# Kernel optimization log

Hardware: AMD Instinct MI355X
Metric: run time of the kernel (lower is better)

The kernel has to match this reference:

```python
import jax, jax.numpy as jnp
import numpy as np

EPS = 1e-05


def layer_norm(x, scale):
    # Faithful to source bug: returns scale * x_norm + scale (shift param unused)
    mean = jnp.mean(x, axis=-1, keepdims=True)
    var = jnp.var(x, axis=-1, keepdims=True)  # unbiased=False
    x_norm = (x - mean) / jnp.sqrt(var + EPS)
    return scale * x_norm + scale


def mhsa(x, wq, wk, wv, wo, bo, n_heads):
    b, t, d = x.shape
    hd = d // n_heads
    # torch Linear: y = x @ W.T (no qkv bias)
    q = (x @ wq.T).reshape(b, t, n_heads, hd).transpose(0, 2, 1, 3)  # bhtd
    k = (x @ wk.T).reshape(b, t, n_heads, hd).transpose(0, 2, 1, 3)
    v = (x @ wv.T).reshape(b, t, n_heads, hd).transpose(0, 2, 1, 3)
    scores = jnp.einsum('bhqd,bhkd->bhqk', q, k)
    causal = jnp.triu(jnp.ones((t, t), dtype=bool), k=1)
    scores = jnp.where(causal, -jnp.inf, scores)
    attn = jax.nn.softmax(scores / np.sqrt(hd).astype(np.float32), axis=-1)
    ctx = jnp.einsum('bhqk,bhkd->bhqd', attn, v)
    ctx = ctx.transpose(0, 2, 1, 3).reshape(b, t, d)
    return ctx @ wo.T + bo


def setup_inputs() -> dict:
    key = jax.random.key(0)
    ks = jax.random.split(key, 6)
    B, T, D = 2, 2048, 1024
    return {
        'x': jax.random.normal(ks[0], (B, T, D), dtype=jnp.float32),
        'wq': jax.random.normal(ks[1], (D, D), dtype=jnp.float32) * 0.02,
        'wk': jax.random.normal(ks[2], (D, D), dtype=jnp.float32) * 0.02,
        'wv': jax.random.normal(ks[3], (D, D), dtype=jnp.float32) * 0.02,
        'wo': jax.random.normal(ks[4], (D, D), dtype=jnp.float32) * 0.02,
        'bo': jnp.zeros((D,), dtype=jnp.float32),
        'ln1_scale': jnp.ones((D,), dtype=jnp.float32),
        'ln2_scale': jnp.ones((D,), dtype=jnp.float32),
    }


def reference(x, wq, wk, wv, wo, bo, ln1_scale, ln2_scale):
    n_heads = 16
    # Block 1: norm1 -> attn -> (+residual); dropout is identity in eval mode
    h = x + mhsa(layer_norm(x, ln1_scale), wq, wk, wv, wo, bo, n_heads)
    # Block 2: source calls self.attn (same weights) again, not self.ff
    out = h + mhsa(layer_norm(h, ln2_scale), wq, wk, wv, wo, bo, n_heads)
    return out
```

## Files before the change

### kernel.cpp

```cpp
#include <hip/hip_runtime.h>
#include <hip/hip_bf16.h>
#include <math.h>

#define Dm 1024
#define Tm 2048
#define Bm 2
#define Hm 16
#define HDm 64
#define Rm (Bm*Tm)
#define QKS 2048

typedef __attribute__((ext_vector_type(8))) short sh8;
typedef __attribute__((ext_vector_type(4))) float f32x4;
typedef __attribute__((ext_vector_type(16))) float f32x16;

#define AS1(p) ((const __attribute__((address_space(1))) void*)(p))
#define AS3(p) ((__attribute__((address_space(3))) void*)(p))

__device__ __forceinline__ short f2bs(float f) {
    union { float f; unsigned u; } v; v.f = f;
    unsigned r = v.u + 0x7FFFu + ((v.u >> 16) & 1u);
    return (short)(r >> 16);
}

__global__ __launch_bounds__(256) void convert_w(const float* __restrict__ wq,
                                                 const float* __restrict__ wk,
                                                 const float* __restrict__ wv,
                                                 const float* __restrict__ wo,
                                                 short* __restrict__ wqkv,
                                                 short* __restrict__ wob) {
    int idx = (blockIdx.x * 256 + threadIdx.x) * 4;
    const int M1 = 1 << 20;
    const float* src; short* dst; int off; float sc = 1.0f;
    if (idx < M1)           { src = wq; dst = wqkv;          off = idx; sc = 0.125f; }
    else if (idx < 2*M1)    { src = wk; dst = wqkv + M1;     off = idx - M1; }
    else if (idx < 3*M1)    { src = wv; dst = wqkv + 2*M1;   off = idx - 2*M1; }
    else                    { src = wo; dst = wob;           off = idx - 3*M1; }
    float4 v = *(const float4*)(src + off);
    short4 o;
    o.x = f2bs(v.x*sc); o.y = f2bs(v.y*sc); o.z = f2bs(v.z*sc); o.w = f2bs(v.w*sc);
    *(short4*)(dst + off) = o;
}

__global__ __launch_bounds__(256) void ln_kernel(const float* __restrict__ x,
                                                 const float* __restrict__ scale,
                                                 short* __restrict__ out) {
    int row = blockIdx.x;
    int t = threadIdx.x;
    const float4* xr = (const float4*)(x + (size_t)row * Dm);
    float4 v = xr[t];
    float s  = v.x + v.y + v.z + v.w;
    float ss = v.x*v.x + v.y*v.y + v.z*v.z + v.w*v.w;
    #pragma unroll
    for (int off = 32; off; off >>= 1) {
        s  += __shfl_xor(s, off);
        ss += __shfl_xor(ss, off);
    }
    __shared__ float red[8];
    int wave = t >> 6, lane = t & 63;
    if (lane == 0) { red[wave*2] = s; red[wave*2+1] = ss; }
    __syncthreads();
    s  = red[0] + red[2] + red[4] + red[6];
    ss = red[1] + red[3] + red[5] + red[7];
    float mean = s * (1.0f / Dm);
    float var  = ss * (1.0f / Dm) - mean * mean;
    float rstd = 1.0f / sqrtf(var + 1e-5f);
    float4 sc = ((const float4*)scale)[t];
    short4 o;
    o.x = f2bs(sc.x * ((v.x - mean) * rstd) + sc.x);
    o.y = f2bs(sc.y * ((v.y - mean) * rstd) + sc.y);
    o.z = f2bs(sc.z * ((v.z - mean) * rstd) + sc.z);
    o.w = f2bs(sc.w * ((v.w - mean) * rstd) + sc.w);
    ((short4*)(out + (size_t)row * Dm))[t] = o;
}

template<int BN, int MODE>
__global__ __launch_bounds__(256) void gemm_mfma(const short* __restrict__ A,
                                                 const short* __restrict__ B,
                                                 const float* __restrict__ bias,
                                                 const float* __restrict__ res,
                                                 void* __restrict__ Cv,
                                                 short* __restrict__ Vt,
                                                 int M, int N, int K) {
    __shared__ short As[128*32];
    __shared__ short Bs[BN*32];
    __shared__ short Tb[(MODE==1) ? 4*16*68 : 4];
    const int NJ = BN / 32;
    int t = threadIdx.x;
    int lane = t & 63, w = t >> 6;
    int l = lane & 15, quad = lane >> 4;
    int wm = (w & 1) * 64, wn = (w >> 1) * (BN/2);
    int m0 = blockIdx.y * 128, n0 = blockIdx.x * BN;

    f32x4 acc[4][NJ];
    #pragma unroll
    for (int i = 0; i < 4; i++)
        #pragma unroll
        for (int j = 0; j < NJ; j++)
            acc[i][j] = (f32x4){0.f,0.f,0.f,0.f};

    for (int k0 = 0; k0 < K; k0 += 32) {
        __syncthreads();
        #pragma unroll
        for (int p = 0; p < 2; p++) {
            int off = p*4096 + t*16;
            int row = off >> 6;
            int c = ((off >> 4) & 3) ^ (row & 3);
            const short* ga = A + (size_t)(m0 + row) * K + k0 + c*8;
            __builtin_amdgcn_global_load_lds(AS1(ga), AS3((char*)As + off), 16, 0, 0);
        }
        #pragma unroll
        for (int p = 0; p < BN/64; p++) {
            int off = p*4096 + t*16;
            int row = off >> 6;
            int c = ((off >> 4) & 3) ^ (row & 3);
            const short* gb = B + (size_t)(n0 + row) * K + k0 + c*8;
            __builtin_amdgcn_global_load_lds(AS1(gb), AS3((char*)Bs + off), 16, 0, 0);
        }
        __syncthreads();
        sh8 af[4], bf[NJ];
        #pragma unroll
        for (int i = 0; i < 4; i++) {
            int m = wm + i*16 + l;
            af[i] = *(const sh8*)((const char*)As + m*64 + ((quad ^ (m & 3)) * 16));
        }
        #pragma unroll
        for (int j = 0; j < NJ; j++) {
            int n = wn + j*16 + l;
            bf[j] = *(const sh8*)((const char*)Bs + n*64 + ((quad ^ (n & 3)) * 16));
        }
        #pragma unroll
        for (int i = 0; i < 4; i++)
            #pragma unroll
            for (int j = 0; j < NJ; j++)
                acc[i][j] = __builtin_amdgcn_mfma_f32_16x16x32_bf16(af[i], bf[j], acc[i][j], 0, 0, 0);
    }
    if (MODE == 0) {
        #pragma unroll
        for (int i = 0; i < 4; i++)
            #pragma unroll
            for (int j = 0; j < NJ; j++)
                #pragma unroll
                for (int r = 0; r < 4; r++) {
                    int m = m0 + wm + i*16 + quad*4 + r;
                    int n = n0 + wn + j*16 + l;
                    float vv = acc[i][j][r] + bias[n] + res[(size_t)m * N + n];
                    ((float*)Cv)[(size_t)m * N + n] = vv;
                }
    } else {
        if (n0 < 2048) {
            #pragma unroll
            for (int i = 0; i < 4; i++)
                #pragma unroll
                for (int j = 0; j < NJ; j++)
                    #pragma unroll
                    for (int r = 0; r < 4; r++) {
                        int m = m0 + wm + i*16 + quad*4 + r;
                        int n = n0 + wn + j*16 + l;
                        ((short*)Cv)[(size_t)m * QKS + n] = f2bs(acc[i][j][r]);
                    }
        } else {
            int bq = m0 >> 11;
            int key0 = (m0 & 2047) + wm;
            int h = (n0 + wn - 2048) >> 6;
            int quad2 = ((quad & 1) << 1) | (quad >> 1);
            short* vout = Vt + ((size_t)(bq*Hm + h) * HDm) * Tm + key0;
            #pragma unroll
            for (int j = 0; j < NJ; j++) {
                #pragma unroll
                for (int i = 0; i < 4; i++) {
                    short4 o;
                    o.x = f2bs(acc[i][j][0]); o.y = f2bs(acc[i][j][1]);
                    o.z = f2bs(acc[i][j][2]); o.w = f2bs(acc[i][j][3]);
                    *(short4*)&Tb[w*(16*68) + l*68 + i*16 + quad2*4] = o;
                }
                #pragma unroll
                for (int st = 0; st < 2; st++) {
                    int rr = st*8 + (lane >> 3);
                    int cc = lane & 7;
                    sh8 vv = *(const sh8*)&Tb[w*(16*68) + rr*68 + cc*8];
                    *(sh8*)(vout + (size_t)(j*16 + rr) * Tm + cc*8) = vv;
                }
            }
        }
    }
}

__global__ __launch_bounds__(256) void attn_mfma(const short* __restrict__ qk,
                                                 const short* __restrict__ vtg,
                                                 short* __restrict__ ctx) {
    __shared__ short Kl[3][64*64];
    __shared__ short Vl[2][64*64];
    int t = threadIdx.x;
    int lane = t & 63, w = t >> 6;
    int qh = w & 1, kh = w >> 1;
    int l31 = lane & 31, hi = lane >> 5;
    int bh = blockIdx.x;
    int xi = blockIdx.y;
    int cc0 = xi & 7, kk0 = xi >> 3;
    int qt = (kk0 == 0) ? cc0 : (kk0 == 1) ? (15 - cc0)
           : (kk0 == 2) ? (16 + cc0) : (31 - cc0);
    int b = bh >> 4, h = bh & 15;
    size_t rbase = (size_t)b * Tm;
    const short* qp0 = qk + rbase * QKS + h*HDm;
    const short* kp0 = qp0 + Dm;
    const short* vh  = vtg + ((size_t)bh * HDm) * Tm;
    int qtbase = qt * 64;
    int qrow = qtbase + qh*32 + l31;

    sh8 qf[4];
    {
        const short* qp = qp0 + (size_t)qrow * QKS + hi*8;
        qf[0] = *(const sh8*)qp;
        qf[1] = *(const sh8*)(qp + 16);
        qf[2] = *(const sh8*)(qp + 32);
        qf[3] = *(const sh8*)(qp + 48);
    }

    f32x16 O0, O1;
    #pragma unroll
    for (int i = 0; i < 16; i++) { O0[i] = 0.f; O1[i] = 0.f; }
    float ps = 0.f;

    int trow = t >> 3;
    int c8 = ((t & 7) ^ (trow & 7)) * 8;
    int ldsoff = t * 16;
    const short* gkp = kp0 + (size_t)trow * QKS + c8;
    const short* gvp = vh + (size_t)trow * Tm + c8;

#define STAGE_K(KD) do { \
    __builtin_amdgcn_global_load_lds(AS1(gkp),                  AS3((char*)(KD) + ldsoff), 16, 0, 0); \
    __builtin_amdgcn_global_load_lds(AS1(gkp + (size_t)32*QKS), AS3((char*)(KD) + 4096 + ldsoff), 16, 0, 0); \
    gkp += (size_t)64*QKS; } while (0)

#define STAGE_V(VD) do { \
    __builtin_amdgcn_global_load_lds(AS1(gvp),                 AS3((char*)(VD) + ldsoff), 16, 0, 0); \
    __builtin_amdgcn_global_load_lds(AS1(gvp + (size_t)32*Tm), AS3((char*)(VD) + 4096 + ldsoff), 16, 0, 0); \
    gvp += 64; } while (0)

#define QKCOMP(KBUF) do { \
    const char* kr_ = (const char*)(KBUF) + (kh*32 + l31)*128; \
    int sw_ = l31 & 7; \
    f32x16 c_; \
    _Pragma("unroll") for (int i_ = 0; i_ < 16; i_++) c_[i_] = 0.f; \
    _Pragma("unroll") for (int s_ = 0; s_ < 4; s_++) { \
        sh8 kf_ = *(const sh8*)(kr_ + (((s_*2 + hi) ^ sw_) * 16)); \
        c_ = __builtin_amdgcn_mfma_f32_32x32x16_bf16(kf_, qf[s_], c_, 0, 0, 0); } \
    S0 = c_; \
} while (0)

    STAGE_K(Kl[0]);
    STAGE_V(Vl[0]);
    if (qt >= 1) STAGE_K(Kl[1]);
    __syncthreads();

    f32x16 S0;
    QKCOMP(Kl[0]);

    int bcur = 0;
    for (int kc = 0; kc <= qt; kc++) {
        int kbase = kc * 64;
        sh8 pa[2];
        {
            bool needmask = (kbase + kh*32 + 31 > qtbase + qh*32);
            float p_[16];
            if (needmask) {
                #pragma unroll
                for (int r = 0; r < 16; r++) {
                    int key_r = kbase + kh*32 + (r&3) + 8*(r>>2) + 4*hi;
                    p_[r] = (key_r > qrow) ? 0.f : __expf(S0[r]);
                }
            } else {
                #pragma unroll
                for (int r = 0; r < 16; r++) p_[r] = __expf(S0[r]);
            }
            ps += (((p_[0]+p_[1])+(p_[2]+p_[3])) + ((p_[4]+p_[5])+(p_[6]+p_[7])))
                + (((p_[8]+p_[9])+(p_[10]+p_[11])) + ((p_[12]+p_[13])+(p_[14]+p_[15])));
            #pragma unroll
            for (int gg = 0; gg < 2; gg++) {
                union { __hip_bfloat162 h2[4]; sh8 s8; } u;
                u.h2[0] = __float22bfloat162_rn({p_[gg*8+0], p_[gg*8+1]});
                u.h2[1] = __float22bfloat162_rn({p_[gg*8+2], p_[gg*8+3]});
                u.h2[2] = __float22bfloat162_rn({p_[gg*8+4], p_[gg*8+5]});
                u.h2[3] = __float22bfloat162_rn({p_[gg*8+6], p_[gg*8+7]});
                pa[gg] = u.s8;
            }
        }

        __syncthreads();

        int bnext = (bcur == 2) ? 0 : bcur + 1;
        if (kc + 2 <= qt) {
            int bnext2 = (bnext == 2) ? 0 : bnext + 1;
            STAGE_K(Kl[bnext2]);
        }
        if (kc + 1 <= qt) STAGE_V(Vl[(kc + 1) & 1]);

        if (kc < qt) QKCOMP(Kl[bnext]);

        const char* Vb = (const char*)Vl[kc & 1];
        int G0 = kh * 2;
        {
            const char* vr = Vb + l31*128;
            int sw = l31 & 7;
            sh8 v0 = *(const sh8*)(vr + ((((G0  )*2 + hi) ^ sw) * 16));
            sh8 v1 = *(const sh8*)(vr + ((((G0+1)*2 + hi) ^ sw) * 16));
            O0 = __builtin_amdgcn_mfma_f32_32x32x16_bf16(pa[0], v0, O0, 0, 0, 0);
            O0 = __builtin_amdgcn_mfma_f32_32x32x16_bf16(pa[1], v1, O0, 0, 0, 0);
        }
        {
            const char* vr = Vb + (32 + l31)*128;
            int sw = l31 & 7;
            sh8 v0 = *(const sh8*)(vr + ((((G0  )*2 + hi) ^ sw) * 16));
            sh8 v1 = *(const sh8*)(vr + ((((G0+1)*2 + hi) ^ sw) * 16));
            O1 = __builtin_amdgcn_mfma_f32_32x32x16_bf16(pa[0], v0, O1, 0, 0, 0);
            O1 = __builtin_amdgcn_mfma_f32_32x32x16_bf16(pa[1], v1, O1, 0, 0, 0);
        }
        bcur = bnext;
    }
#undef STAGE_K
#undef STAGE_V
#undef QKCOMP

    ps += __shfl_xor(ps, 32);
    __syncthreads();
    float* Lo  = (float*)Kl;
    float* Lps = (float*)Vl;
    if (kh == 1) {
        #pragma unroll
        for (int r = 0; r < 16; r++) {
            int rl = (r&3) + 8*(r>>2) + 4*hi;
            Lo[qh*2048 + rl*64 + l31]      = O0[r];
            Lo[qh*2048 + rl*64 + 32 + l31] = O1[r];
        }
        if (hi == 0) Lps[qh*32 + l31] = ps;
    }
    __syncthreads();
    if (kh == 0) {
        float pst = ps + Lps[qh*32 + l31];
        float inv_own = 1.0f / pst;
        short* cp = ctx + (rbase + qtbase + qh*32) * Dm + h*HDm + l31;
        #pragma unroll
        for (int r = 0; r < 16; r++) {
            int rl = (r&3) + 8*(r>>2) + 4*hi;
            float inv = __shfl(inv_own, rl);
            cp[(size_t)rl * Dm]      = f2bs((O0[r] + Lo[qh*2048 + rl*64 + l31]) * inv);
            cp[(size_t)rl * Dm + 32] = f2bs((O1[r] + Lo[qh*2048 + rl*64 + 32 + l31]) * inv);
        }
    }
}

extern "C" void kernel_launch(void* const* d_in, const int* in_sizes, int n_in,
                              void* d_out, int out_size, void* d_ws, size_t ws_size,
                              hipStream_t stream) {
    const float* x   = (const float*)d_in[0];
    const float* wq  = (const float*)d_in[1];
    const float* wk  = (const float*)d_in[2];
    const float* wv  = (const float*)d_in[3];
    const float* wo  = (const float*)d_in[4];
    const float* bo  = (const float*)d_in[5];
    const float* ln1 = (const float*)d_in[6];
    const float* ln2 = (const float*)d_in[7];
    float* out = (float*)d_out;

    short* lnb  = (short*)d_ws;
    short* ctxb = lnb  + (size_t)Rm*Dm;
    short* qk   = ctxb + (size_t)Rm*Dm;
    short* vtg  = qk   + (size_t)Rm*QKS;
    short* wqkv = vtg  + (size_t)Bm*Hm*HDm*Tm;
    short* wob  = wqkv + (size_t)3*Dm*Dm;

    dim3 qgrid(3072/128, Rm/128);
    dim3 pgrid(Dm/64,    Rm/128);
    dim3 agrid(32, 32);

    convert_w<<<4096, 256, 0, stream>>>(wq, wk, wv, wo, wqkv, wob);

    ln_kernel<<<Rm, 256, 0, stream>>>(x, ln1, lnb);
    gemm_mfma<128, 1><<<qgrid, 256, 0, stream>>>(lnb, wqkv, nullptr, nullptr, qk, vtg, Rm, 3072, Dm);
    attn_mfma<<<agrid, 256, 0, stream>>>(qk, vtg, ctxb);
    gemm_mfma<64, 0><<<pgrid, 256, 0, stream>>>(ctxb, wob, bo, x, out, nullptr, Rm, Dm, Dm);

    ln_kernel<<<Rm, 256, 0, stream>>>(out, ln2, lnb);
    gemm_mfma<128, 1><<<qgrid, 256, 0, stream>>>(lnb, wqkv, nullptr, nullptr, qk, vtg, Rm, 3072, Dm);
    attn_mfma<<<agrid, 256, 0, stream>>>(qk, vtg, ctxb);
    gemm_mfma<64, 0><<<pgrid, 256, 0, stream>>>(ctxb, wob, bo, out, out, nullptr, Rm, Dm, Dm);
}
```

Measured before the change: 284.6 us.

## Double GEMM K-tile to 64 and fuse weight conversion into first layernorm

Each GEMM k-step now stages 64 K-elements instead of 32, with an 8-way XOR swizzle on 128-byte LDS rows. This halves the number of barrier pairs and loop iterations per tile, and each wave issues two MFMAs per fragment pair. The weight-to-bf16 conversion kernel is merged into the first layernorm launch as extra blocks, removing one kernel launch and letting the two independent jobs overlap. In exchange, LDS use per block roughly doubles, which may lower occupancy.

```diff
diff --git a/kernel.cpp b/kernel.cpp
--- a/kernel.cpp
+++ b/kernel.cpp
@@ -23,23 +23,56 @@
     return (short)(r >> 16);
 }
 
-__global__ __launch_bounds__(256) void convert_w(const float* __restrict__ wq,
-                                                 const float* __restrict__ wk,
-                                                 const float* __restrict__ wv,
-                                                 const float* __restrict__ wo,
-                                                 short* __restrict__ wqkv,
-                                                 short* __restrict__ wob) {
-    int idx = (blockIdx.x * 256 + threadIdx.x) * 4;
-    const int M1 = 1 << 20;
-    const float* src; short* dst; int off; float sc = 1.0f;
-    if (idx < M1)           { src = wq; dst = wqkv;          off = idx; sc = 0.125f; }
-    else if (idx < 2*M1)    { src = wk; dst = wqkv + M1;     off = idx - M1; }
-    else if (idx < 3*M1)    { src = wv; dst = wqkv + 2*M1;   off = idx - 2*M1; }
-    else                    { src = wo; dst = wob;           off = idx - 3*M1; }
-    float4 v = *(const float4*)(src + off);
+__global__ __launch_bounds__(256) void ln_conv(const float* __restrict__ x,
+                                               const float* __restrict__ scale,
+                                               short* __restrict__ out,
+                                               const float* __restrict__ wq,
+                                               const float* __restrict__ wk,
+                                               const float* __restrict__ wv,
+                                               const float* __restrict__ wo,
+                                               short* __restrict__ wqkv,
+                                               short* __restrict__ wob) {
+    __shared__ float red[8];
+    if (blockIdx.x >= 4096) {
+        int idx = ((blockIdx.x - 4096) * 256 + threadIdx.x) * 4;
+        const int M1 = 1 << 20;
+        const float* src; short* dst; int off; float sc = 1.0f;
+        if (idx < M1)           { src = wq; dst = wqkv;          off = idx; sc = 0.125f; }
+        else if (idx < 2*M1)    { src = wk; dst = wqkv + M1;     off = idx - M1; }
+        else if (idx < 3*M1)    { src = wv; dst = wqkv + 2*M1;   off = idx - 2*M1; }
+        else                    { src = wo; dst = wob;           off = idx - 3*M1; }
+        float4 v = *(const float4*)(src + off);
+        short4 o;
+        o.x = f2bs(v.x*sc); o.y = f2bs(v.y*sc); o.z = f2bs(v.z*sc); o.w = f2bs(v.w*sc);
+        *(short4*)(dst + off) = o;
+        return;
+    }
+    int row = blockIdx.x;
+    int t = threadIdx.x;
+    const float4* xr = (const float4*)(x + (size_t)row * Dm);
+    float4 v = xr[t];
+    float s  = v.x + v.y + v.z + v.w;
+    float ss = v.x*v.x + v.y*v.y + v.z*v.z + v.w*v.w;
+    #pragma unroll
+    for (int off = 32; off; off >>= 1) {
+        s  += __shfl_xor(s, off);
+        ss += __shfl_xor(ss, off);
+    }
+    int wave = t >> 6, lane = t & 63;
+    if (lane == 0) { red[wave*2] = s; red[wave*2+1] = ss; }
+    __syncthreads();
+    s  = red[0] + red[2] + red[4] + red[6];
+    ss = red[1] + red[3] + red[5] + red[7];
+    float mean = s * (1.0f / Dm);
+    float var  = ss * (1.0f / Dm) - mean * mean;
+    float rstd = 1.0f / sqrtf(var + 1e-5f);
+    float4 sc = ((const float4*)scale)[t];
     short4 o;
-    o.x = f2bs(v.x*sc); o.y = f2bs(v.y*sc); o.z = f2bs(v.z*sc); o.w = f2bs(v.w*sc);
-    *(short4*)(dst + off) = o;
+    o.x = f2bs(sc.x * ((v.x - mean) * rstd) + sc.x);
+    o.y = f2bs(sc.y * ((v.y - mean) * rstd) + sc.y);
+    o.z = f2bs(sc.z * ((v.z - mean) * rstd) + sc.z);
+    o.w = f2bs(sc.w * ((v.w - mean) * rstd) + sc.w);
+    ((short4*)(out + (size_t)row * Dm))[t] = o;
 }
 
 __global__ __launch_bounds__(256) void ln_kernel(const float* __restrict__ x,
@@ -82,8 +115,8 @@
                                                  void* __restrict__ Cv,
                                                  short* __restrict__ Vt,
                                                  int M, int N, int K) {
-    __shared__ short As[128*32];
-    __shared__ short Bs[BN*32];
+    __shared__ short As[128*64];
+    __shared__ short Bs[BN*64];
     __shared__ short Tb[(MODE==1) ? 4*16*68 : 4];
     const int NJ = BN / 32;
     int t = threadIdx.x;
@@ -99,41 +132,49 @@
         for (int j = 0; j < NJ; j++)
             acc[i][j] = (f32x4){0.f,0.f,0.f,0.f};
 
-    for (int k0 = 0; k0 < K; k0 += 32) {
+    for (int k0 = 0; k0 < K; k0 += 64) {
         __syncthreads();
         #pragma unroll
-        for (int p = 0; p < 2; p++) {
+        for (int p = 0; p < 4; p++) {
             int off = p*4096 + t*16;
-            int row = off >> 6;
-            int c = ((off >> 4) & 3) ^ (row & 3);
+            int row = off >> 7;
+            int c = ((off >> 4) & 7) ^ (row & 7);
             const short* ga = A + (size_t)(m0 + row) * K + k0 + c*8;
             __builtin_amdgcn_global_load_lds(AS1(ga), AS3((char*)As + off), 16, 0, 0);
         }
         #pragma unroll
-        for (int p = 0; p < BN/64; p++) {
+        for (int p = 0; p < BN/32; p++) {
             int off = p*4096 + t*16;
-            int row = off >> 6;
-            int c = ((off >> 4) & 3) ^ (row & 3);
+            int row = off >> 7;
+            int c = ((off >> 4) & 7) ^ (row & 7);
             const short* gb = B + (size_t)(n0 + row) * K + k0 + c*8;
             __builtin_amdgcn_global_load_lds(AS1(gb), AS3((char*)Bs + off), 16, 0, 0);
         }
         __syncthreads();
-        sh8 af[4], bf[NJ];
+        sh8 a0[4], a1[4], b0[NJ], b1[NJ];
         #pragma unroll
         for (int i = 0; i < 4; i++) {
             int m = wm + i*16 + l;
-            af[i] = *(const sh8*)((const char*)As + m*64 + ((quad ^ (m & 3)) * 16));
+            const char* ar = (const char*)As + m*128;
+            int sw = m & 7;
+            a0[i] = *(const sh8*)(ar + ((quad ^ sw) * 16));
+            a1[i] = *(const sh8*)(ar + (((4 + quad) ^ sw) * 16));
         }
         #pragma unroll
         for (int j = 0; j < NJ; j++) {
             int n = wn + j*16 + l;
-            bf[j] = *(const sh8*)((const char*)Bs + n*64 + ((quad ^ (n & 3)) * 16));
+            const char* br = (const char*)Bs + n*128;
+            int sw = n & 7;
+            b0[j] = *(const sh8*)(br + ((quad ^ sw) * 16));
+            b1[j] = *(const sh8*)(br + (((4 + quad) ^ sw) * 16));
         }
         #pragma unroll
         for (int i = 0; i < 4; i++)
             #pragma unroll
-            for (int j = 0; j < NJ; j++)
-                acc[i][j] = __builtin_amdgcn_mfma_f32_16x16x32_bf16(af[i], bf[j], acc[i][j], 0, 0, 0);
+            for (int j = 0; j < NJ; j++) {
+                acc[i][j] = __builtin_amdgcn_mfma_f32_16x16x32_bf16(a0[i], b0[j], acc[i][j], 0, 0, 0);
+                acc[i][j] = __builtin_amdgcn_mfma_f32_16x16x32_bf16(a1[i], b1[j], acc[i][j], 0, 0, 0);
+            }
     }
     if (MODE == 0) {
         #pragma unroll
@@ -374,9 +415,7 @@
     dim3 pgrid(Dm/64,    Rm/128);
     dim3 agrid(32, 32);
 
-    convert_w<<<4096, 256, 0, stream>>>(wq, wk, wv, wo, wqkv, wob);
-
-    ln_kernel<<<Rm, 256, 0, stream>>>(x, ln1, lnb);
+    ln_conv<<<8192, 256, 0, stream>>>(x, ln1, lnb, wq, wk, wv, wo, wqkv, wob);
     gemm_mfma<128, 1><<<qgrid, 256, 0, stream>>>(lnb, wqkv, nullptr, nullptr, qk, vtg, Rm, 3072, Dm);
     attn_mfma<<<agrid, 256, 0, stream>>>(qk, vtg, ctxb);
     gemm_mfma<64, 0><<<pgrid, 256, 0, stream>>>(ctxb, wob, bo, x, out, nullptr, Rm, Dm, Dm);
```

Result: faster. 266.8 us (median of 2 runs) (-6.3%).
